# Kernel tuning notes

Measured on AMD Instinct MI355X. Metric: run time of the kernel, lower is better.

Reference implementation:

```python
import jax, jax.numpy as jnp
import numpy as np
from jax import lax

NQ = 9          # num_qubits
K = 3           # basis_size
S = 16          # max_num_snapshots
H = 128         # hidden_size
B = 16          # batch
D = 2 ** NQ

# basis_reconstruction buffer = Pauli X, Y, Z (complex64), non-trainable
PAULI = jnp.array([[[0, 1], [1, 0]],
                   [[0, -1j], [1j, 0]],
                   [[1, 0], [0, -1]]], dtype=jnp.complex64)


def setup_inputs() -> dict:
    key = jax.random.key(0)
    ks = jax.random.split(key, 11)
    return {
        "snapshot": jax.random.normal(ks[0], (B, NQ), jnp.float32),
        "basis_comp_vector": jax.random.uniform(ks[1], (B, NQ, K), dtype=jnp.float32),
        "rho": jax.random.normal(ks[2], (B, 2) + (2,) * NQ, jnp.float32),
        "h0": jax.random.normal(ks[3], (B, H), jnp.float32),
        "c0": jax.random.normal(ks[4], (B, H), jnp.float32),
        "W_ih": jax.random.normal(ks[5], (4 * H, NQ + NQ * K), jnp.float32) * 0.1,
        "W_hh": jax.random.normal(ks[6], (4 * H, H), jnp.float32) * 0.1,
        "b_ih": jax.random.normal(ks[7], (4 * H,), jnp.float32) * 0.1,
        "b_hh": jax.random.normal(ks[8], (4 * H,), jnp.float32) * 0.1,
        "Wp": jax.random.normal(ks[9], (NQ, K, H), jnp.float32) * 0.1,
        "bp": jax.random.normal(ks[10], (NQ, K), jnp.float32) * 0.1,
    }


def _lstm_cell(x, h, c, W_ih, W_hh, b_ih, b_hh):
    g = x @ W_ih.T + h @ W_hh.T + b_ih + b_hh
    i, f, gg, o = jnp.split(g, 4, axis=-1)  # torch gate order i,f,g,o
    i, f, o = jax.nn.sigmoid(i), jax.nn.sigmoid(f), jax.nn.sigmoid(o)
    c = f * c + i * jnp.tanh(gg)
    return o * jnp.tanh(c), c


def _apply_1q(psi, M, i):
    """Apply per-batch 2x2 matrix M [B,2,2] to qubit i of psi [B]+[2]*NQ."""
    psi = jnp.moveaxis(psi, 1 + i, 1)
    sh = psi.shape
    out = jnp.einsum('bij,bjr->bir', M, psi.reshape(sh[0], 2, -1))
    return jnp.moveaxis(out.reshape(sh), 1, 1 + i)


def _take_snapshots(psi, a):
    """Vectorized take_snapshot: psi [B]+[2]*NQ complex, a [B,NQ,K] real (sqrt of probs).
    For each qubit build psi_plus/psi_minus projectors, record expectation
    s = <P+> - <P-> and collapse onto the (normalized) plus branch."""
    axs = tuple(range(1, NQ + 1))
    zeros = jnp.zeros(psi.shape[0], jnp.float32)
    ss = []
    for i in range(NQ):
        a1, a2, a3 = a[:, i, 0], a[:, i, 1], a[:, i, 2]
        an = jnp.sqrt(a1 * a1 + a2 * a2 + a3 * a3)
        nrm = 1.0 / jnp.sqrt(2.0 * an * (a3 + an))
        pp = jnp.stack([lax.complex(a3 + an, zeros), lax.complex(a1, a2)], axis=-1) * nrm[:, None]
        pm = jnp.stack([lax.complex(-a1, a2), lax.complex(a3 + an, zeros)], axis=-1) * nrm[:, None]
        Pp = pp[:, :, None] * jnp.conj(pp)[:, None, :]  # [B,2,2]
        Pm = pm[:, :, None] * jnp.conj(pm)[:, None, :]
        psi_p = _apply_1q(psi, Pp, i)
        psi_m = _apply_1q(psi, Pm, i)
        prob_p = jnp.sum(psi_p.real ** 2 + psi_p.imag ** 2, axis=axs)
        prob_m = jnp.sum(psi_m.real ** 2 + psi_m.imag ** 2, axis=axs)
        ss.append(prob_p - prob_m)
        psi = psi_p / jnp.sqrt(prob_p).reshape((-1,) + (1,) * NQ)  # collapse
    return jnp.stack(ss, axis=1)  # [B,NQ]


def _bkron(A, Bm):
    b, m, n = A.shape
    p, q = Bm.shape[1], Bm.shape[2]
    return (A[:, :, None, :, None] * Bm[:, None, :, None, :]).reshape(b, m * p, n * q)


def _forward(snapshot, basis_comp_vector, rho, h0, c0, W_ih, W_hh, b_ih, b_hh, Wp, bp):
    b = snapshot.shape[0]
    psi = lax.complex(rho[:, 0], rho[:, 1])  # [B]+[2]*NQ pure state
    x = jnp.concatenate([snapshot, basis_comp_vector.reshape(b, -1)], axis=-1)
    inputs = [x]
    h, c = h0, c0
    for _ in range(S - 1):
        h, c = _lstm_cell(x, h, c, W_ih, W_hh, b_ih, b_hh)
        probs = jax.nn.softmax(jnp.einsum('bh,nkh->bnk', h, Wp) + bp, axis=-1)
        amps = jnp.sqrt(probs)  # [B,NQ,K]
        snap = _take_snapshots(psi, amps)
        x = jnp.concatenate([snap, amps.reshape(b, -1)], axis=-1)
        inputs.append(x)
    # classical-shadow reconstruction, summed over snapshots
    I2 = jnp.eye(2, dtype=jnp.complex64)
    acc = jnp.zeros((b, D, D), jnp.complex64)
    last_bv = None
    for x in inputs:
        shadow = x[:, :NQ]                                   # [B,NQ]
        bv = x[:, NQ:].reshape(b, NQ, K)
        last_bv = bv
        basis = jnp.einsum('bnk,kij->bnij', bv.astype(jnp.complex64), PAULI)
        rho_q = (I2 + shadow[:, :, None, None].astype(jnp.complex64) * basis * 3.0) / 2.0
        r = rho_q[:, 0]
        for iq in range(1, NQ):
            r = _bkron(r, rho_q[:, iq])
        acc = acc + r
    rho_rec = acc / S
    out = jnp.stack([rho_rec.real, rho_rec.imag], axis=1)  # [B,2,D,D]
    return out, last_bv


def reference(snapshot, basis_comp_vector, rho, h0, c0, W_ih, W_hh, b_ih, b_hh, Wp, bp):
    return _forward(snapshot, basis_comp_vector, rho, h0, c0,
                    W_ih, W_hh, b_ih, b_hh, Wp, bp)
```

## Files before the change

kernel.cpp:

```cpp
#include <hip/hip_runtime.h>
#include <math.h>

#define NQ 9
#define KK 3
#define S 16
#define H 128
#define BB 16
#define D 512
#define DD (D*D)

typedef float vfloat4 __attribute__((ext_vector_type(4)));

__device__ __forceinline__ float sigf(float x){ return 1.f/(1.f + __expf(-x)); }
__device__ __forceinline__ float tanhfast(float x){
  float e = __expf(2.f*x);
  return 1.f - 2.f/(e + 1.f);
}
#define RCP(x)  __builtin_amdgcn_rcpf(x)
#define RSQ(x)  __builtin_amdgcn_rsqf(x)

#define DPP_ADD(x, ctrl, rmask) \
  x += __int_as_float(__builtin_amdgcn_update_dpp(0, __float_as_int(x), ctrl, rmask, 0xf, false))

__device__ __forceinline__ float wave_red_sum(float x) {
  DPP_ADD(x, 0x111, 0xf);
  DPP_ADD(x, 0x112, 0xf);
  DPP_ADD(x, 0x114, 0xf);
  DPP_ADD(x, 0x118, 0xf);
  DPP_ADD(x, 0x142, 0xa);
  DPP_ADD(x, 0x143, 0xc);
  return __int_as_float(__builtin_amdgcn_readlane(__float_as_int(x), 63));
}
#define RL(v, l) __int_as_float(__builtin_amdgcn_readlane(__float_as_int(v), (l)))
#define DPP_ROR(x, n) \
  __int_as_float(__builtin_amdgcn_update_dpp(0, __float_as_int(x), 0x120 + (n), 0xf, 0xf, false))

__global__ __launch_bounds__(512, 2)
void seq_kernel(const float* __restrict__ snapshot,
                const float* __restrict__ bcv,
                const float* __restrict__ rho,
                const float* __restrict__ h0,
                const float* __restrict__ c0,
                const float* __restrict__ W_ih,
                const float* __restrict__ W_hh,
                const float* __restrict__ b_ih,
                const float* __restrict__ b_hh,
                const float* __restrict__ Wp,
                const float* __restrict__ bp,
                float4* __restrict__ mats,
                float* __restrict__ last_bv)
{
  const int b    = blockIdx.x;
  const int tid  = threadIdx.x;
  const int lane = tid & 63;
  const int w    = tid >> 6;

  __shared__ __align__(16) float xh[36];
  __shared__ float gbuf[512];
  __shared__ float prj[27];

  float4 wih[9], whh[32];
  {
    const float4* wi = (const float4*)(W_ih + tid*36);
    #pragma unroll
    for (int k = 0; k < 9; ++k) wih[k] = wi[k];
    const float4* wh = (const float4*)(W_hh + tid*H);
    #pragma unroll
    for (int k = 0; k < 32; ++k) whh[k] = wh[k];
  }
  const float bias = b_ih[tid] + b_hh[tid];
  float2 wpv[4]; float bpv[4];
  #pragma unroll
  for (int i = 0; i < 4; ++i) {
    int u = w + 8*i;
    if (u < 27) { wpv[i] = *(const float2*)(Wp + u*H + 2*lane); bpv[i] = bp[u]; }
    else        { wpv[i] = make_float2(0.f, 0.f); bpv[i] = 0.f; }
  }

  float cc0 = c0[b*H + 2*lane], cc1 = c0[b*H + 2*lane + 1];
  float h0v = h0[b*H + 2*lane], h1v = h0[b*H + 2*lane + 1];

  float pr0[8], pi0[8], norm0 = 0.f;
  if (w == 0) {
    #pragma unroll
    for (int j = 0; j < 8; ++j) {
      pr0[j] = rho[b*1024 + j*64 + lane];
      pi0[j] = rho[b*1024 + 512 + j*64 + lane];
    }
    float ls = 0.f;
    #pragma unroll
    for (int j = 0; j < 8; ++j) ls += pr0[j]*pr0[j] + pi0[j]*pi0[j];
    norm0 = wave_red_sum(ls);
  }

  if (tid < NQ)  xh[tid]      = snapshot[b*NQ + tid];
  if (tid < 27)  xh[NQ + tid] = bcv[b*27 + tid];
  if (tid < NQ) {
    float s  = snapshot[b*NQ + tid];
    float v0 = bcv[b*27 + tid*3];
    float v1 = bcv[b*27 + tid*3 + 1];
    float v2 = bcv[b*27 + tid*3 + 2];
    mats[(b*S + 0)*NQ + tid] = make_float4(
        0.5f*(1.f + 3.f*s*v2), 1.5f*s*v0, -1.5f*s*v1, 0.5f*(1.f - 3.f*s*v2));
  }

  float ghh = bias;
  #pragma unroll
  for (int j = 0; j < 32; ++j) {
    float4 wv = whh[j];
    ghh += wv.x*RL(h0v, 2*j)     + wv.y*RL(h1v, 2*j)
         + wv.z*RL(h0v, 2*j + 1) + wv.w*RL(h1v, 2*j + 1);
  }
  __syncthreads();

  for (int t = 1; t < S; ++t) {
    {
      const float4* x4 = (const float4*)xh;
      float g0 = ghh, g1 = 0.f, g2 = 0.f, g3 = 0.f;
      #pragma unroll
      for (int k = 0; k < 9; ++k) {
        float4 wv = wih[k], xv = x4[k];
        g0 += wv.x*xv.x; g1 += wv.y*xv.y; g2 += wv.z*xv.z; g3 += wv.w*xv.w;
      }
      gbuf[tid] = (g0 + g1) + (g2 + g3);
    }
    __syncthreads();

    {
      float2 gI = *(const float2*)(gbuf + 2*lane);
      float2 gF = *(const float2*)(gbuf + 128 + 2*lane);
      float2 gG = *(const float2*)(gbuf + 256 + 2*lane);
      float2 gO = *(const float2*)(gbuf + 384 + 2*lane);
      cc0 = sigf(gF.x)*cc0 + sigf(gI.x)*tanhfast(gG.x);
      cc1 = sigf(gF.y)*cc1 + sigf(gI.y)*tanhfast(gG.y);
      h0v = sigf(gO.x)*tanhfast(cc0);
      h1v = sigf(gO.y)*tanhfast(cc1);
    }
    #pragma unroll
    for (int i = 0; i < 4; ++i) {
      float p = wave_red_sum(wpv[i].x*h0v + wpv[i].y*h1v);
      int u = w + 8*i;
      if (u < 27 && lane == 0) prj[u] = p + bpv[i];
    }
    __syncthreads();

    if (w == 0) {
      float a1 = 0.f, a2 = 0.f, a3 = 0.f;
      float k0v = 0.f, k1rv = 0.f, k1iv = 0.f;
      if (lane < NQ) {
        float l0 = prj[lane*3], l1 = prj[lane*3+1], l2 = prj[lane*3+2];
        float mx = fmaxf(l0, fmaxf(l1, l2));
        float e0 = __expf(l0 - mx), e1 = __expf(l1 - mx), e2 = __expf(l2 - mx);
        float inv = RCP(e0 + e1 + e2);
        a1 = sqrtf(e0*inv); a2 = sqrtf(e1*inv); a3 = sqrtf(e2*inv);
        float an = sqrtf(a1*a1 + a2*a2 + a3*a3);
        float t3 = a3 + an;
        float n1 = RSQ(2.f*an*t3);
        k0v = n1*t3; k1rv = n1*a1; k1iv = -n1*a2;
      }
      float part[9];

      float r4[4], i4[4];
      {
        const float K0 = RL(k0v,0), K1r = RL(k1rv,0), K1i = RL(k1iv,0);
        float lp = 0.f;
        #pragma unroll
        for (int j = 0; j < 4; ++j) {
          r4[j] = K0*pr0[j] + K1r*pr0[j+4] - K1i*pi0[j+4];
          i4[j] = K0*pi0[j] + K1r*pi0[j+4] + K1i*pr0[j+4];
          lp += r4[j]*r4[j] + i4[j]*i4[j];
        }
        part[0] = lp;
      }
      float r2[2], i2[2];
      {
        const float K0 = RL(k0v,1), K1r = RL(k1rv,1), K1i = RL(k1iv,1);
        float lp = 0.f;
        #pragma unroll
        for (int j = 0; j < 2; ++j) {
          r2[j] = K0*r4[j] + K1r*r4[j+2] - K1i*i4[j+2];
          i2[j] = K0*i4[j] + K1r*i4[j+2] + K1i*r4[j+2];
          lp += r2[j]*r2[j] + i2[j]*i2[j];
        }
        part[1] = lp;
      }
      float wr, wi_;
      {
        const float K0 = RL(k0v,2), K1r = RL(k1rv,2), K1i = RL(k1iv,2);
        wr  = K0*r2[0] + K1r*r2[1] - K1i*i2[1];
        wi_ = K0*i2[0] + K1r*i2[1] + K1i*r2[1];
        part[2] = wr*wr + wi_*wi_;
      }
      #pragma unroll
      for (int q = 3; q < 5; ++q) {
        const int half = 32 >> (q - 3);
        const float K0 = RL(k0v,q), K1r = RL(k1rv,q), K1i = RL(k1iv,q);
        float pr = __shfl(wr,  lane + half, 64);
        float pi = __shfl(wi_, lane + half, 64);
        float nr = K0*wr  + K1r*pr - K1i*pi;
        float ni = K0*wi_ + K1r*pi + K1i*pr;
        wr = nr; wi_ = ni;
        part[q] = (lane < half) ? (nr*nr + ni*ni) : 0.f;
      }
      #pragma unroll
      for (int q = 5; q < NQ; ++q) {
        const int half = 32 >> (q - 3);
        const float K0 = RL(k0v,q), K1r = RL(k1rv,q), K1i = RL(k1iv,q);
        float pr, pi;
        if      (q == 5) { pr = DPP_ROR(wr, 8);  pi = DPP_ROR(wi_, 8);  }
        else if (q == 6) { pr = DPP_ROR(wr, 12); pi = DPP_ROR(wi_, 12); }
        else if (q == 7) { pr = DPP_ROR(wr, 14); pi = DPP_ROR(wi_, 14); }
        else             { pr = DPP_ROR(wr, 15); pi = DPP_ROR(wi_, 15); }
        float nr = K0*wr  + K1r*pr - K1i*pi;
        float ni = K0*wi_ + K1r*pi + K1i*pr;
        wr = nr; wi_ = ni;
        part[q] = (lane < half) ? (nr*nr + ni*ni) : 0.f;
      }
      float L[9];
      #pragma unroll
      for (int q = 0; q < NQ; ++q) L[q] = wave_red_sum(part[q]);
      float sv = 2.f*L[0] - norm0;
      #pragma unroll
      for (int q = 1; q < NQ; ++q) {
        float r = 2.f*L[q]*RCP(L[q-1]) - 1.f;
        sv = (lane == q) ? r : sv;
      }
      if (lane < NQ) {
        xh[lane] = sv;
        xh[9 + lane*3]     = a1;
        xh[9 + lane*3 + 1] = a2;
        xh[9 + lane*3 + 2] = a3;
        mats[(b*S + t)*NQ + lane] = make_float4(
            0.5f*(1.f + 3.f*sv*a3), 1.5f*sv*a1,
            -1.5f*sv*a2,            0.5f*(1.f - 3.f*sv*a3));
      }
    }

    if (t < S - 1) {
      float g = bias;
      #pragma unroll
      for (int j = 0; j < 32; ++j) {
        float4 wv = whh[j];
        g += wv.x*RL(h0v, 2*j)     + wv.y*RL(h1v, 2*j)
           + wv.z*RL(h0v, 2*j + 1) + wv.w*RL(h1v, 2*j + 1);
      }
      ghh = g;
    }
    __syncthreads();
  }

  if (tid < 27) last_bv[b*27 + tid] = xh[9 + tid];
}

__device__ __forceinline__ void herm_entry(float4 m, int rb, int cb, float& er, float& ei) {
  if (rb == 0) { if (cb == 0) { er = m.x; ei = 0.f; } else { er = m.y; ei = m.z; } }
  else         { if (cb == 0) { er = m.y; ei = -m.z; } else { er = m.w; ei = 0.f; } }
}

__device__ __forceinline__ void nt_store4(float* p, float x, float y, float z, float w) {
  vfloat4 v; v.x = x; v.y = y; v.z = z; v.w = w;
  __builtin_nontemporal_store(v, (vfloat4*)p);
}

__global__ __launch_bounds__(512, 2)
void kron_kernel(const float4* __restrict__ mats_g, float* __restrict__ out)
{
  const int b   = blockIdx.y;
  const int bm  = blockIdx.x;
  const int tid = threadIdx.x;
  const int rTp = bm >> 3;
  const int rg  = bm & 7;

  __shared__ float4 matsh[S*NQ];
  __shared__ float2 top[S][2][16];
  __shared__ __align__(16) float2 bot[4][S][32];

  if (tid < S*NQ) matsh[tid] = mats_g[b*S*NQ + tid];
  __syncthreads();

  {
    int t = tid >> 5, rTi = (tid >> 4) & 1, cT = tid & 15;
    int rT = rTp*2 + rTi;
    float re = 1.f, im = 0.f;
    #pragma unroll
    for (int q = 0; q < 4; ++q) {
      int rb = (rT >> (3 - q)) & 1, cb = (cT >> (3 - q)) & 1;
      float er, ei; herm_entry(matsh[t*NQ + q], rb, cb, er, ei);
      float nr = re*er - im*ei; im = re*ei + im*er; re = nr;
    }
    top[t][rTi][cT] = make_float2(re, im);
  }
  #pragma unroll
  for (int i = 0; i < 4; ++i) {
    int n  = tid + 512*i;
    int r_ = n >> 9, t_ = (n >> 5) & 15, cB = n & 31;
    int rB = rg*4 + r_;
    float re = 1.f, im = 0.f;
    #pragma unroll
    for (int q = 0; q < 5; ++q) {
      int rb = (rB >> (4 - q)) & 1, cb = (cB >> (4 - q)) & 1;
      float er, ei; herm_entry(matsh[t_*NQ + 4 + q], rb, cb, er, ei);
      float nr = re*er - im*ei; im = re*ei + im*er; re = nr;
    }
    bot[r_][t_][cB] = make_float2(re, im);
  }
  __syncthreads();

  const int rb = tid >> 7;
  const int c0 = (tid & 127) << 2;
  const int cT = c0 >> 5, cB = c0 & 31;
  float4 a0r = make_float4(0,0,0,0), a0i = make_float4(0,0,0,0);
  float4 a1r = make_float4(0,0,0,0), a1i = make_float4(0,0,0,0);
  #pragma unroll
  for (int t = 0; t < S; ++t) {
    float4 b01 = *(const float4*)&bot[rb][t][cB];
    float4 b23 = *(const float4*)&bot[rb][t][cB + 2];
    float2 tA = top[t][0][cT];
    float2 tB = top[t][1][cT];
    a0r.x += tA.x*b01.x - tA.y*b01.y;  a0i.x += tA.x*b01.y + tA.y*b01.x;
    a0r.y += tA.x*b01.z - tA.y*b01.w;  a0i.y += tA.x*b01.w + tA.y*b01.z;
    a0r.z += tA.x*b23.x - tA.y*b23.y;  a0i.z += tA.x*b23.y + tA.y*b23.x;
    a0r.w += tA.x*b23.z - tA.y*b23.w;  a0i.w += tA.x*b23.w + tA.y*b23.z;
    a1r.x += tB.x*b01.x - tB.y*b01.y;  a1i.x += tB.x*b01.y + tB.y*b01.x;
    a1r.y += tB.x*b01.z - tB.y*b01.w;  a1i.y += tB.x*b01.w + tB.y*b01.z;
    a1r.z += tB.x*b23.x - tB.y*b23.y;  a1i.z += tB.x*b23.y + tB.y*b23.x;
    a1r.w += tB.x*b23.z - tB.y*b23.w;  a1i.w += tB.x*b23.w + tB.y*b23.z;
  }
  const float invS = 1.f/16.f;
  const int rowA = (rTp*2)*32 + rg*4 + rb;
  const int rowB = rowA + 32;
  size_t baseA = ((size_t)b*2)*DD + (size_t)rowA*D + c0;
  size_t baseB = ((size_t)b*2)*DD + (size_t)rowB*D + c0;
  nt_store4(out + baseA,      a0r.x*invS, a0r.y*invS, a0r.z*invS, a0r.w*invS);
  nt_store4(out + baseA + DD, a0i.x*invS, a0i.y*invS, a0i.z*invS, a0i.w*invS);
  nt_store4(out + baseB,      a1r.x*invS, a1r.y*invS, a1r.z*invS, a1r.w*invS);
  nt_store4(out + baseB + DD, a1i.x*invS, a1i.y*invS, a1i.z*invS, a1i.w*invS);
}

extern "C" void kernel_launch(void* const* d_in, const int* in_sizes, int n_in,
                              void* d_out, int out_size, void* d_ws, size_t ws_size,
                              hipStream_t stream) {
  const float* snapshot = (const float*)d_in[0];
  const float* bcv      = (const float*)d_in[1];
  const float* rho      = (const float*)d_in[2];
  const float* h0       = (const float*)d_in[3];
  const float* c0       = (const float*)d_in[4];
  const float* W_ih     = (const float*)d_in[5];
  const float* W_hh     = (const float*)d_in[6];
  const float* b_ih     = (const float*)d_in[7];
  const float* b_hh     = (const float*)d_in[8];
  const float* Wp       = (const float*)d_in[9];
  const float* bp       = (const float*)d_in[10];

  float*  out     = (float*)d_out;
  float4* mats    = (float4*)d_ws;
  float*  last_bv = out + (size_t)BB*2*DD;

  seq_kernel<<<BB, 512, 0, stream>>>(snapshot, bcv, rho, h0, c0,
                                     W_ih, W_hh, b_ih, b_hh, Wp, bp,
                                     mats, last_bv);

  dim3 grid(64, BB);
  kron_kernel<<<grid, 512, 0, stream>>>(mats, out);
}
```

Baseline: 155.3 us.

## Overlap hidden-state and amplitude gate terms with wave-0 snapshot simulation

Wave 0 no longer computes its own W_hh·h and amplitude part of W_ih·x. Wave 7 computes those terms for wave 0's gate rows and passes them through shared memory. The amplitudes are published before the snapshot simulation behind an extra barrier, so waves 1-7 can precompute the next step's gate terms while wave 0 runs the serial snapshot chain. Only the 9 snapshot terms are left on the critical path. Wave 7 now holds a second copy of its weights in registers, so launch bounds drop to one block per SM, and each step gains an extra barrier.

```diff
diff --git a/kernel.cpp b/kernel.cpp
--- a/kernel.cpp
+++ b/kernel.cpp
@@ -35,7 +35,42 @@
 #define DPP_ROR(x, n) \
   __int_as_float(__builtin_amdgcn_update_dpp(0, __float_as_int(x), 0x120 + (n), 0xf, 0xf, false))
 
-__global__ __launch_bounds__(512, 2)
+__device__ __forceinline__ float ghh_rl(const float4 (&whh)[32],
+                                        float h0v, float h1v, float bias) {
+  float g = bias;
+  #pragma unroll
+  for (int j = 0; j < 32; ++j) {
+    float4 wv = whh[j];
+    g += wv.x*RL(h0v, 2*j)     + wv.y*RL(h1v, 2*j)
+       + wv.z*RL(h0v, 2*j + 1) + wv.w*RL(h1v, 2*j + 1);
+  }
+  return g;
+}
+
+__device__ __forceinline__ float ampsdot(const float4 (&wih)[9], const float* xh) {
+  const float4* x4 = (const float4*)xh;
+  float4 w2 = wih[2], v2 = x4[2];
+  float a = w2.y*v2.y + w2.z*v2.z + w2.w*v2.w;
+  #pragma unroll
+  for (int k = 3; k < 9; ++k) {
+    float4 wv = wih[k], xv = x4[k];
+    a += wv.x*xv.x + wv.y*xv.y + wv.z*xv.z + wv.w*xv.w;
+  }
+  return a;
+}
+__device__ __forceinline__ float ampsdot2(const float4 (&wih2)[7], const float* xh) {
+  const float4* x4 = (const float4*)xh;
+  float4 w2 = wih2[0], v2 = x4[2];
+  float a = w2.y*v2.y + w2.z*v2.z + w2.w*v2.w;
+  #pragma unroll
+  for (int k = 1; k < 7; ++k) {
+    float4 wv = wih2[k], xv = x4[k + 2];
+    a += wv.x*xv.x + wv.y*xv.y + wv.z*xv.z + wv.w*xv.w;
+  }
+  return a;
+}
+
+__global__ __launch_bounds__(512, 1)
 void seq_kernel(const float* __restrict__ snapshot,
                 const float* __restrict__ bcv,
                 const float* __restrict__ rho,
@@ -58,6 +93,7 @@
   __shared__ __align__(16) float xh[36];
   __shared__ float gbuf[512];
   __shared__ float prj[27];
+  __shared__ float prebuf[64];
 
   float4 wih[9], whh[32];
   {
@@ -69,6 +105,19 @@
     for (int k = 0; k < 32; ++k) whh[k] = wh[k];
   }
   const float bias = b_ih[tid] + b_hh[tid];
+
+  float4 wih2[7], whh2[32];
+  float bias2 = 0.f;
+  if (w == 7) {
+    const float4* wi2 = (const float4*)(W_ih + lane*36);
+    #pragma unroll
+    for (int k = 0; k < 7; ++k) wih2[k] = wi2[k + 2];
+    const float4* wh2 = (const float4*)(W_hh + lane*H);
+    #pragma unroll
+    for (int k = 0; k < 32; ++k) whh2[k] = wh2[k];
+    bias2 = b_ih[lane] + b_hh[lane];
+  }
+
   float2 wpv[4]; float bpv[4];
   #pragma unroll
   for (int i = 0; i < 4; ++i) {
@@ -103,26 +152,27 @@
     mats[(b*S + 0)*NQ + tid] = make_float4(
         0.5f*(1.f + 3.f*s*v2), 1.5f*s*v0, -1.5f*s*v1, 0.5f*(1.f - 3.f*s*v2));
   }
-
-  float ghh = bias;
-  #pragma unroll
-  for (int j = 0; j < 32; ++j) {
-    float4 wv = whh[j];
-    ghh += wv.x*RL(h0v, 2*j)     + wv.y*RL(h1v, 2*j)
-         + wv.z*RL(h0v, 2*j + 1) + wv.w*RL(h1v, 2*j + 1);
+  __syncthreads();
+
+  float pre = 0.f;
+  if (w > 0) {
+    pre = ghh_rl(whh, h0v, h1v, bias) + ampsdot(wih, xh);
+    if (w == 7)
+      prebuf[lane] = ghh_rl(whh2, h0v, h1v, bias2) + ampsdot2(wih2, xh);
   }
   __syncthreads();
 
   for (int t = 1; t < S; ++t) {
     {
       const float4* x4 = (const float4*)xh;
-      float g0 = ghh, g1 = 0.f, g2 = 0.f, g3 = 0.f;
-      #pragma unroll
-      for (int k = 0; k < 9; ++k) {
-        float4 wv = wih[k], xv = x4[k];
-        g0 += wv.x*xv.x; g1 += wv.y*xv.y; g2 += wv.z*xv.z; g3 += wv.w*xv.w;
-      }
-      gbuf[tid] = (g0 + g1) + (g2 + g3);
+      float myPre = (w == 0) ? prebuf[lane] : pre;
+      float4 s0 = x4[0], s1 = x4[1];
+      float s8 = x4[2].x;
+      float g = myPre
+              + wih[0].x*s0.x + wih[0].y*s0.y + wih[0].z*s0.z + wih[0].w*s0.w
+              + wih[1].x*s1.x + wih[1].y*s1.y + wih[1].z*s1.z + wih[1].w*s1.w
+              + wih[2].x*s8;
+      gbuf[tid] = g;
     }
     __syncthreads();
 
@@ -144,9 +194,9 @@
     }
     __syncthreads();
 
+    float a1 = 0.f, a2 = 0.f, a3 = 0.f;
+    float k0v = 0.f, k1rv = 0.f, k1iv = 0.f;
     if (w == 0) {
-      float a1 = 0.f, a2 = 0.f, a3 = 0.f;
-      float k0v = 0.f, k1rv = 0.f, k1iv = 0.f;
       if (lane < NQ) {
         float l0 = prj[lane*3], l1 = prj[lane*3+1], l2 = prj[lane*3+2];
         float mx = fmaxf(l0, fmaxf(l1, l2));
@@ -157,7 +207,14 @@
         float t3 = a3 + an;
         float n1 = RSQ(2.f*an*t3);
         k0v = n1*t3; k1rv = n1*a1; k1iv = -n1*a2;
-      }
+        xh[9 + lane*3]     = a1;
+        xh[9 + lane*3 + 1] = a2;
+        xh[9 + lane*3 + 2] = a3;
+      }
+    }
+    __syncthreads();
+
+    if (w == 0) {
       float part[9];
 
       float r4[4], i4[4];
@@ -227,24 +284,14 @@
       }
       if (lane < NQ) {
         xh[lane] = sv;
-        xh[9 + lane*3]     = a1;
-        xh[9 + lane*3 + 1] = a2;
-        xh[9 + lane*3 + 2] = a3;
         mats[(b*S + t)*NQ + lane] = make_float4(
             0.5f*(1.f + 3.f*sv*a3), 1.5f*sv*a1,
             -1.5f*sv*a2,            0.5f*(1.f - 3.f*sv*a3));
       }
-    }
-
-    if (t < S - 1) {
-      float g = bias;
-      #pragma unroll
-      for (int j = 0; j < 32; ++j) {
-        float4 wv = whh[j];
-        g += wv.x*RL(h0v, 2*j)     + wv.y*RL(h1v, 2*j)
-           + wv.z*RL(h0v, 2*j + 1) + wv.w*RL(h1v, 2*j + 1);
-      }
-      ghh = g;
+    } else if (t < S - 1) {
+      pre = ghh_rl(whh, h0v, h1v, bias) + ampsdot(wih, xh);
+      if (w == 7)
+        prebuf[lane] = ghh_rl(whh2, h0v, h1v, bias2) + ampsdot2(wih2, xh);
     }
     __syncthreads();
   }
```

Result: slower. 288.8 us (+85.9%).

## Overlap hidden-state matvec with snapshot work across waves in LSTM loop

Applied to the files above, without the earlier changes.

Reassigns work in the sequential LSTM kernel. Waves 1-7 now do the projection reductions, and wave 0 computes its W_hh·h matvec during that phase. Waves 1-7 then compute their matvec while wave 0 runs the snapshot/collapse chain, so the recurrent matvec overlaps with the serial work instead of following it. Wave 0 keeps its snapshot and amplitude values in registers and builds its W_ih·x input term with readlane instead of shared memory. The matvec uses four accumulators for more ILP, and launch bounds drop to one block per CU to allow more registers.

```diff
diff --git a/kernel.cpp b/kernel.cpp
--- a/kernel.cpp
+++ b/kernel.cpp
@@ -35,7 +35,25 @@
 #define DPP_ROR(x, n) \
   __int_as_float(__builtin_amdgcn_update_dpp(0, __float_as_int(x), 0x120 + (n), 0xf, 0xf, false))
 
-__global__ __launch_bounds__(512, 2)
+__device__ __forceinline__ float ghh_rl4(const float4 (&whh)[32],
+                                         float h0v, float h1v, float bias) {
+  float g0 = bias, g1 = 0.f, g2 = 0.f, g3 = 0.f;
+  #pragma unroll
+  for (int j = 0; j < 32; ++j) {
+    float4 wv = whh[j];
+    g0 += wv.x*RL(h0v, 2*j);
+    g1 += wv.y*RL(h1v, 2*j);
+    g2 += wv.z*RL(h0v, 2*j + 1);
+    g3 += wv.w*RL(h1v, 2*j + 1);
+  }
+  return (g0 + g1) + (g2 + g3);
+}
+
+#define WIHC(c) ( (((c)&3)==0) ? wih[(c)>>2].x : \
+                  (((c)&3)==1) ? wih[(c)>>2].y : \
+                  (((c)&3)==2) ? wih[(c)>>2].z : wih[(c)>>2].w )
+
+__global__ __launch_bounds__(512, 1)
 void seq_kernel(const float* __restrict__ snapshot,
                 const float* __restrict__ bcv,
                 const float* __restrict__ rho,
@@ -69,10 +87,11 @@
     for (int k = 0; k < 32; ++k) whh[k] = wh[k];
   }
   const float bias = b_ih[tid] + b_hh[tid];
+
   float2 wpv[4]; float bpv[4];
   #pragma unroll
   for (int i = 0; i < 4; ++i) {
-    int u = w + 8*i;
+    int u = (w >= 1) ? (w - 1) + 7*i : 99;
     if (u < 27) { wpv[i] = *(const float2*)(Wp + u*H + 2*lane); bpv[i] = bp[u]; }
     else        { wpv[i] = make_float2(0.f, 0.f); bpv[i] = 0.f; }
   }
@@ -91,6 +110,14 @@
     #pragma unroll
     for (int j = 0; j < 8; ++j) ls += pr0[j]*pr0[j] + pi0[j]*pi0[j];
     norm0 = wave_red_sum(ls);
+  }
+
+  float svr = 0.f, a1r = 0.f, a2r = 0.f, a3r = 0.f;
+  if (w == 0 && lane < NQ) {
+    svr = snapshot[b*NQ + lane];
+    a1r = bcv[b*27 + lane*3];
+    a2r = bcv[b*27 + lane*3 + 1];
+    a3r = bcv[b*27 + lane*3 + 2];
   }
 
   if (tid < NQ)  xh[tid]      = snapshot[b*NQ + tid];
@@ -103,18 +130,22 @@
     mats[(b*S + 0)*NQ + tid] = make_float4(
         0.5f*(1.f + 3.f*s*v2), 1.5f*s*v0, -1.5f*s*v1, 0.5f*(1.f - 3.f*s*v2));
   }
-
-  float ghh = bias;
-  #pragma unroll
-  for (int j = 0; j < 32; ++j) {
-    float4 wv = whh[j];
-    ghh += wv.x*RL(h0v, 2*j)     + wv.y*RL(h1v, 2*j)
-         + wv.z*RL(h0v, 2*j + 1) + wv.w*RL(h1v, 2*j + 1);
-  }
   __syncthreads();
 
+  float ghh = ghh_rl4(whh, h0v, h1v, bias);
+
   for (int t = 1; t < S; ++t) {
-    {
+    if (w == 0) {
+      float g0 = ghh, g1 = 0.f, g2 = 0.f, g3 = 0.f;
+      #pragma unroll
+      for (int q = 0; q < 9; ++q) {
+        g0 += WIHC(q)        * RL(svr, q);
+        g1 += WIHC(9 + 3*q)  * RL(a1r, q);
+        g2 += WIHC(10 + 3*q) * RL(a2r, q);
+        g3 += WIHC(11 + 3*q) * RL(a3r, q);
+      }
+      gbuf[tid] = (g0 + g1) + (g2 + g3);
+    } else {
       const float4* x4 = (const float4*)xh;
       float g0 = ghh, g1 = 0.f, g2 = 0.f, g3 = 0.f;
       #pragma unroll
@@ -136,83 +167,88 @@
       h0v = sigf(gO.x)*tanhfast(cc0);
       h1v = sigf(gO.y)*tanhfast(cc1);
     }
-    #pragma unroll
-    for (int i = 0; i < 4; ++i) {
-      float p = wave_red_sum(wpv[i].x*h0v + wpv[i].y*h1v);
-      int u = w + 8*i;
-      if (u < 27 && lane == 0) prj[u] = p + bpv[i];
+    if (w > 0) {
+      #pragma unroll
+      for (int i = 0; i < 4; ++i) {
+        float p = wave_red_sum(wpv[i].x*h0v + wpv[i].y*h1v);
+        int u = (w - 1) + 7*i;
+        if (u < 27 && lane == 0) prj[u] = p + bpv[i];
+      }
+    } else if (t < S - 1) {
+      ghh = ghh_rl4(whh, h0v, h1v, bias);
     }
     __syncthreads();
 
     if (w == 0) {
-      float a1 = 0.f, a2 = 0.f, a3 = 0.f;
       float k0v = 0.f, k1rv = 0.f, k1iv = 0.f;
       if (lane < NQ) {
         float l0 = prj[lane*3], l1 = prj[lane*3+1], l2 = prj[lane*3+2];
         float mx = fmaxf(l0, fmaxf(l1, l2));
         float e0 = __expf(l0 - mx), e1 = __expf(l1 - mx), e2 = __expf(l2 - mx);
         float inv = RCP(e0 + e1 + e2);
-        a1 = sqrtf(e0*inv); a2 = sqrtf(e1*inv); a3 = sqrtf(e2*inv);
-        float an = sqrtf(a1*a1 + a2*a2 + a3*a3);
-        float t3 = a3 + an;
+        a1r = sqrtf(e0*inv); a2r = sqrtf(e1*inv); a3r = sqrtf(e2*inv);
+        float an = sqrtf(a1r*a1r + a2r*a2r + a3r*a3r);
+        float t3 = a3r + an;
         float n1 = RSQ(2.f*an*t3);
-        k0v = n1*t3; k1rv = n1*a1; k1iv = -n1*a2;
+        k0v = n1*t3; k1rv = n1*a1r; k1iv = -n1*a2r;
+      }
+      float K0a[9], K1ra[9], K1ia[9];
+      #pragma unroll
+      for (int q = 0; q < NQ; ++q) {
+        K0a[q]  = RL(k0v,  q);
+        K1ra[q] = RL(k1rv, q);
+        K1ia[q] = RL(k1iv, q);
       }
       float part[9];
 
       float r4[4], i4[4];
       {
-        const float K0 = RL(k0v,0), K1r = RL(k1rv,0), K1i = RL(k1iv,0);
         float lp = 0.f;
         #pragma unroll
         for (int j = 0; j < 4; ++j) {
-          r4[j] = K0*pr0[j] + K1r*pr0[j+4] - K1i*pi0[j+4];
-          i4[j] = K0*pi0[j] + K1r*pi0[j+4] + K1i*pr0[j+4];
+          r4[j] = K0a[0]*pr0[j] + K1ra[0]*pr0[j+4] - K1ia[0]*pi0[j+4];
+          i4[j] = K0a[0]*pi0[j] + K1ra[0]*pi0[j+4] + K1ia[0]*pr0[j+4];
           lp += r4[j]*r4[j] + i4[j]*i4[j];
         }
         part[0] = lp;
       }
       float r2[2], i2[2];
       {
-        const float K0 = RL(k0v,1), K1r = RL(k1rv,1), K1i = RL(k1iv,1);
         float lp = 0.f;
         #pragma unroll
         for (int j = 0; j < 2; ++j) {
-          r2[j] = K0*r4[j] + K1r*r4[j+2] - K1i*i4[j+2];
-          i2[j] = K0*i4[j] + K1r*i4[j+2] + K1i*r4[j+2];
+          r2[j] = K0a[1]*r4[j] + K1ra[1]*r4[j+2] - K1ia[1]*i4[j+2];
+          i2[j] = K0a[1]*i4[j] + K1ra[1]*i4[j+2] + K1ia[1]*r4[j+2];
           lp += r2[j]*r2[j] + i2[j]*i2[j];
         }
         part[1] = lp;
       }
       float wr, wi_;
       {
-        const float K0 = RL(k0v,2), K1r = RL(k1rv,2), K1i = RL(k1iv,2);
-        wr  = K0*r2[0] + K1r*r2[1] - K1i*i2[1];
-        wi_ = K0*i2[0] + K1r*i2[1] + K1i*r2[1];
+        wr  = K0a[2]*r2[0] + K1ra[2]*r2[1] - K1ia[2]*i2[1];
+        wi_ = K0a[2]*i2[0] + K1ra[2]*i2[1] + K1ia[2]*r2[1];
         part[2] = wr*wr + wi_*wi_;
       }
       #pragma unroll
       for (int q = 3; q < 5; ++q) {
         const int half = 32 >> (q - 3);
-        const float K0 = RL(k0v,q), K1r = RL(k1rv,q), K1i = RL(k1iv,q);
         float pr = __shfl(wr,  lane + half, 64);
         float pi = __shfl(wi_, lane + half, 64);
-        float nr = K0*wr  + K1r*pr - K1i*pi;
-        float ni = K0*wi_ + K1r*pi + K1i*pr;
+        float nr = K0a[q]*wr  + K1ra[q]*pr - K1ia[q]*pi;
+        float ni = K0a[q]*wi_ + K1ra[q]*pi + K1ia[q]*pr;
         wr = nr; wi_ = ni;
         part[q] = (lane < half) ? (nr*nr + ni*ni) : 0.f;
       }
       #pragma unroll
       for (int q = 5; q < NQ; ++q) {
         const int half = 32 >> (q - 3);
-        const float K0 = RL(k0v,q), K1r = RL(k1rv,q), K1i = RL(k1iv,q);
         float pr, pi;
         if      (q == 5) { pr = DPP_ROR(wr, 8);  pi = DPP_ROR(wi_, 8);  }
         else if (q == 6) { pr = DPP_ROR(wr, 12); pi = DPP_ROR(wi_, 12); }
         else if (q == 7) { pr = DPP_ROR(wr, 14); pi = DPP_ROR(wi_, 14); }
         else             { pr = DPP_ROR(wr, 15); pi = DPP_ROR(wi_, 15); }
-        float nr = K0*wr  + K1r*pr - K1i*pi;
-        float ni = K0*wi_ + K1r*pi + K1i*pr;
+        float nr = K0a[q]*wr  + K1ra[q]*pr - K1ia[q]*pi;
+        float ni = K0a[q]*wi_ + K1ra[q]*pi + K1ia[q]*pr;
         wr = nr; wi_ = ni;
         part[q] = (lane < half) ? (nr*nr + ni*ni) : 0.f;
       }
@@ -225,26 +261,18 @@
         float r = 2.f*L[q]*RCP(L[q-1]) - 1.f;
         sv = (lane == q) ? r : sv;
       }
+      svr = sv;
       if (lane < NQ) {
         xh[lane] = sv;
-        xh[9 + lane*3]     = a1;
-        xh[9 + lane*3 + 1] = a2;
-        xh[9 + lane*3 + 2] = a3;
+        xh[9 + lane*3]     = a1r;
+        xh[9 + lane*3 + 1] = a2r;
+        xh[9 + lane*3 + 2] = a3r;
         mats[(b*S + t)*NQ + lane] = make_float4(
-            0.5f*(1.f + 3.f*sv*a3), 1.5f*sv*a1,
-            -1.5f*sv*a2,            0.5f*(1.f - 3.f*sv*a3));
-      }
-    }
-
-    if (t < S - 1) {
-      float g = bias;
-      #pragma unroll
-      for (int j = 0; j < 32; ++j) {
-        float4 wv = whh[j];
-        g += wv.x*RL(h0v, 2*j)     + wv.y*RL(h1v, 2*j)
-           + wv.z*RL(h0v, 2*j + 1) + wv.w*RL(h1v, 2*j + 1);
-      }
-      ghh = g;
+            0.5f*(1.f + 3.f*sv*a3r), 1.5f*sv*a1r,
+            -1.5f*sv*a2r,            0.5f*(1.f - 3.f*sv*a3r));
+      }
+    } else if (t < S - 1) {
+      ghh = ghh_rl4(whh, h0v, h1v, bias);
     }
     __syncthreads();
   }
```

New measurement: 158.4 us. +2.0%, slower.

## Overlap next-step hidden matvec with snapshot collapse using idle waves

Applied to the files above, without the earlier changes.

Wave 0 runs the serial state-collapse chain while waves 1-7 precompute the next step's hidden-to-gate contribution, so the W_hh matvec no longer sits on wave 0's critical path. Gate rows 0-63 are handled by staging their W_hh and basis-amplitude W_ih weights in LDS and splitting the dot products across the seven idle waves, which wave 0 then sums. The softmax/amplitude computation moves into a separate phase before the collapse, which adds an extra block barrier per step. The recurrent matvec accumulator is also split four ways for more ILP. It costs about 41 KB of LDS, which may reduce occupancy.

```diff
diff --git a/kernel.cpp b/kernel.cpp
--- a/kernel.cpp
+++ b/kernel.cpp
@@ -34,6 +34,20 @@
 #define RL(v, l) __int_as_float(__builtin_amdgcn_readlane(__float_as_int(v), (l)))
 #define DPP_ROR(x, n) \
   __int_as_float(__builtin_amdgcn_update_dpp(0, __float_as_int(x), 0x120 + (n), 0xf, 0xf, false))
+
+__device__ __forceinline__ float ghh_rl4(const float4 (&whh)[32],
+                                         float h0v, float h1v, float bias) {
+  float g0 = bias, g1 = 0.f, g2 = 0.f, g3 = 0.f;
+  #pragma unroll
+  for (int j = 0; j < 32; ++j) {
+    float4 wv = whh[j];
+    g0 += wv.x*RL(h0v, 2*j);
+    g1 += wv.y*RL(h1v, 2*j);
+    g2 += wv.z*RL(h0v, 2*j + 1);
+    g3 += wv.w*RL(h1v, 2*j + 1);
+  }
+  return (g0 + g1) + (g2 + g3);
+}
 
 __global__ __launch_bounds__(512, 2)
 void seq_kernel(const float* __restrict__ snapshot,
@@ -58,6 +72,9 @@
   __shared__ __align__(16) float xh[36];
   __shared__ float gbuf[512];
   __shared__ float prj[27];
+  __shared__ float wrow[64][161];
+  __shared__ float hx[161];
+  __shared__ float part[7][64];
 
   float4 wih[9], whh[32];
   {
@@ -92,6 +109,22 @@
     for (int j = 0; j < 8; ++j) ls += pr0[j]*pr0[j] + pi0[j]*pi0[j];
     norm0 = wave_red_sum(ls);
   }
+
+  for (int idx = tid; idx < 64*128; idx += 512) {
+    int r = idx >> 7, c = idx & 127;
+    wrow[r][c] = W_hh[r*H + c];
+  }
+  for (int idx = tid; idx < 64*27; idx += 512) {
+    int r = idx / 27, k = idx - r*27;
+    wrow[r][128 + k] = W_ih[r*36 + 9 + k];
+  }
+  for (int idx = tid; idx < 64*6; idx += 512) {
+    int r = idx / 6, k = idx - r*6;
+    wrow[r][155 + k] = 0.f;
+  }
+  if (tid < 6) hx[155 + tid] = 0.f;
+  if (tid < H)  hx[tid]       = h0[b*H + tid];
+  if (tid < 27) hx[128 + tid] = bcv[b*27 + tid];
 
   if (tid < NQ)  xh[tid]      = snapshot[b*NQ + tid];
   if (tid < 27)  xh[NQ + tid] = bcv[b*27 + tid];
@@ -103,18 +136,38 @@
     mats[(b*S + 0)*NQ + tid] = make_float4(
         0.5f*(1.f + 3.f*s*v2), 1.5f*s*v0, -1.5f*s*v1, 0.5f*(1.f - 3.f*s*v2));
   }
-
-  float ghh = bias;
-  #pragma unroll
-  for (int j = 0; j < 32; ++j) {
-    float4 wv = whh[j];
-    ghh += wv.x*RL(h0v, 2*j)     + wv.y*RL(h1v, 2*j)
-         + wv.z*RL(h0v, 2*j + 1) + wv.w*RL(h1v, 2*j + 1);
-  }
   __syncthreads();
 
+  float ghh = 0.f;
+  if (w > 0) {
+    ghh = ghh_rl4(whh, h0v, h1v, bias);
+    const int ht = tid - 64;
+    const int r = ht & 63, j = ht >> 6;
+    const float* wr_ = &wrow[r][j*23];
+    const float* hx_ = &hx[j*23];
+    float acc0 = 0.f, acc1 = 0.f;
+    #pragma unroll
+    for (int k = 0; k < 23; k += 2) {
+      acc0 += wr_[k] * hx_[k];
+      if (k + 1 < 23) acc1 += wr_[k+1] * hx_[k+1];
+    }
+    part[j][r] = acc0 + acc1;
+  }
+  __syncthreads();
+
   for (int t = 1; t < S; ++t) {
-    {
+    if (w == 0) {
+      float g = bias;
+      #pragma unroll
+      for (int j = 0; j < 7; ++j) g += part[j][lane];
+      const float4* x4 = (const float4*)xh;
+      float4 s0 = x4[0], s1 = x4[1];
+      float s8 = ((const float*)xh)[8];
+      g += wih[0].x*s0.x + wih[0].y*s0.y + wih[0].z*s0.z + wih[0].w*s0.w
+         + wih[1].x*s1.x + wih[1].y*s1.y + wih[1].z*s1.z + wih[1].w*s1.w
+         + wih[2].x*s8;
+      gbuf[tid] = g;
+    } else {
       const float4* x4 = (const float4*)xh;
       float g0 = ghh, g1 = 0.f, g2 = 0.f, g3 = 0.f;
       #pragma unroll
@@ -135,6 +188,7 @@
       cc1 = sigf(gF.y)*cc1 + sigf(gI.y)*tanhfast(gG.y);
       h0v = sigf(gO.x)*tanhfast(cc0);
       h1v = sigf(gO.y)*tanhfast(cc1);
+      if (w == 1) *(float2*)(hx + 2*lane) = make_float2(h0v, h1v);
     }
     #pragma unroll
     for (int i = 0; i < 4; ++i) {
@@ -144,21 +198,29 @@
     }
     __syncthreads();
 
+    float a1 = 0.f, a2 = 0.f, a3 = 0.f;
+    float k0v = 0.f, k1rv = 0.f, k1iv = 0.f;
+    if (w == 0 && lane < NQ) {
+      float l0 = prj[lane*3], l1 = prj[lane*3+1], l2 = prj[lane*3+2];
+      float mx = fmaxf(l0, fmaxf(l1, l2));
+      float e0 = __expf(l0 - mx), e1 = __expf(l1 - mx), e2 = __expf(l2 - mx);
+      float inv = RCP(e0 + e1 + e2);
+      a1 = sqrtf(e0*inv); a2 = sqrtf(e1*inv); a3 = sqrtf(e2*inv);
+      float an = sqrtf(a1*a1 + a2*a2 + a3*a3);
+      float t3 = a3 + an;
+      float n1 = RSQ(2.f*an*t3);
+      k0v = n1*t3; k1rv = n1*a1; k1iv = -n1*a2;
+      xh[9 + lane*3]      = a1;
+      xh[9 + lane*3 + 1]  = a2;
+      xh[9 + lane*3 + 2]  = a3;
+      hx[128 + lane*3]     = a1;
+      hx[128 + lane*3 + 1] = a2;
+      hx[128 + lane*3 + 2] = a3;
+    }
+    __syncthreads();
+
     if (w == 0) {
-      float a1 = 0.f, a2 = 0.f, a3 = 0.f;
-      float k0v = 0.f, k1rv = 0.f, k1iv = 0.f;
-      if (lane < NQ) {
-        float l0 = prj[lane*3], l1 = prj[lane*3+1], l2 = prj[lane*3+2];
-        float mx = fmaxf(l0, fmaxf(l1, l2));
-        float e0 = __expf(l0 - mx), e1 = __expf(l1 - mx), e2 = __expf(l2 - mx);
-        float inv = RCP(e0 + e1 + e2);
-        a1 = sqrtf(e0*inv); a2 = sqrtf(e1*inv); a3 = sqrtf(e2*inv);
-        float an = sqrtf(a1*a1 + a2*a2 + a3*a3);
-        float t3 = a3 + an;
-        float n1 = RSQ(2.f*an*t3);
-        k0v = n1*t3; k1rv = n1*a1; k1iv = -n1*a2;
-      }
-      float part[9];
+      float part9[9];
 
       float r4[4], i4[4];
       {
@@ -170,7 +232,7 @@
           i4[j] = K0*pi0[j] + K1r*pi0[j+4] + K1i*pr0[j+4];
           lp += r4[j]*r4[j] + i4[j]*i4[j];
         }
-        part[0] = lp;
+        part9[0] = lp;
       }
       float r2[2], i2[2];
       {
@@ -182,14 +244,14 @@
           i2[j] = K0*i4[j] + K1r*i4[j+2] + K1i*r4[j+2];
           lp += r2[j]*r2[j] + i2[j]*i2[j];
         }
-        part[1] = lp;
+        part9[1] = lp;
       }
       float wr, wi_;
       {
         const float K0 = RL(k0v,2), K1r = RL(k1rv,2), K1i = RL(k1iv,2);
         wr  = K0*r2[0] + K1r*r2[1] - K1i*i2[1];
         wi_ = K0*i2[0] + K1r*i2[1] + K1i*r2[1];
-        part[2] = wr*wr + wi_*wi_;
+        part9[2] = wr*wr + wi_*wi_;
       }
       #pragma unroll
       for (int q = 3; q < 5; ++q) {
@@ -200,7 +262,7 @@
         float nr = K0*wr  + K1r*pr - K1i*pi;
         float ni = K0*wi_ + K1r*pi + K1i*pr;
         wr = nr; wi_ = ni;
-        part[q] = (lane < half) ? (nr*nr + ni*ni) : 0.f;
+        part9[q] = (lane < half) ? (nr*nr + ni*ni) : 0.f;
       }
       #pragma unroll
       for (int q = 5; q < NQ; ++q) {
@@ -214,11 +276,11 @@
         float nr = K0*wr  + K1r*pr - K1i*pi;
         float ni = K0*wi_ + K1r*pi + K1i*pr;
         wr = nr; wi_ = ni;
-        part[q] = (lane < half) ? (nr*nr + ni*ni) : 0.f;
+        part9[q] = (lane < half) ? (nr*nr + ni*ni) : 0.f;
       }
       float L[9];
       #pragma unroll
-      for (int q = 0; q < NQ; ++q) L[q] = wave_red_sum(part[q]);
+      for (int q = 0; q < NQ; ++q) L[q] = wave_red_sum(part9[q]);
       float sv = 2.f*L[0] - norm0;
       #pragma unroll
       for (int q = 1; q < NQ; ++q) {
@@ -227,24 +289,23 @@
       }
       if (lane < NQ) {
         xh[lane] = sv;
-        xh[9 + lane*3]     = a1;
-        xh[9 + lane*3 + 1] = a2;
-        xh[9 + lane*3 + 2] = a3;
         mats[(b*S + t)*NQ + lane] = make_float4(
             0.5f*(1.f + 3.f*sv*a3), 1.5f*sv*a1,
             -1.5f*sv*a2,            0.5f*(1.f - 3.f*sv*a3));
       }
-    }
-
-    if (t < S - 1) {
-      float g = bias;
-      #pragma unroll
-      for (int j = 0; j < 32; ++j) {
-        float4 wv = whh[j];
-        g += wv.x*RL(h0v, 2*j)     + wv.y*RL(h1v, 2*j)
-           + wv.z*RL(h0v, 2*j + 1) + wv.w*RL(h1v, 2*j + 1);
-      }
-      ghh = g;
+    } else if (t < S - 1) {
+      ghh = ghh_rl4(whh, h0v, h1v, bias);
+      const int ht = tid - 64;
+      const int r = ht & 63, j = ht >> 6;
+      const float* wr_ = &wrow[r][j*23];
+      const float* hx_ = &hx[j*23];
+      float acc0 = 0.f, acc1 = 0.f;
+      #pragma unroll
+      for (int k = 0; k < 23; k += 2) {
+        acc0 += wr_[k] * hx_[k];
+        if (k + 1 < 23) acc1 += wr_[k+1] * hx_[k+1];
+      }
+      part[j][r] = acc0 + acc1;
     }
     __syncthreads();
   }
```

Result: slower. 174.8 us (+12.6%).
